# Kernel optimization log

Hardware: AMD Instinct MI355X
Metric: run time of the kernel (lower is better)

## Reference

```python
import jax, jax.numpy as jnp
import numpy as np
import math

N_NODES, CHANNELS, N_ELEM, N_FEAT = 4096, 128, 10, 128
LS_IN = [0, 1, 2]          # input irreps per channel: 0e+1o+2e -> dim 9
L_OUT = [0, 1]             # keep_irrep_out = {0e, 1o}
L12_MAX = 3                # cap on intermediate coupling
SLICES = {0: (0, 1), 1: (1, 4), 2: (4, 9)}
PATHS1 = [l for l in L_OUT if l in LS_IN]
PATHS2 = [(l1, l2, lo) for l1 in LS_IN for l2 in LS_IN for lo in L_OUT if abs(l1 - l2) <= lo <= l1 + l2]
T12_KEYS = [(l1, l2, l12) for l1 in LS_IN for l2 in LS_IN for l12 in range(abs(l1 - l2), min(l1 + l2, L12_MAX) + 1)]
PATHS3 = [(k, l3, lo) for k in T12_KEYS for l3 in LS_IN for lo in L_OUT if abs(k[2] - l3) <= lo <= k[2] + l3]

def _su2_cg(j1, m1, j2, m2, j3, m3):
    if m3 != m1 + m2:
        return 0.0
    f = math.factorial
    vmin = max(-j1 + j2 + m3, -j1 + m1, 0)
    vmax = min(j2 + j3 + m1, j3 - j1 + j2, j3 + m3)
    C = math.sqrt((2 * j3 + 1) * f(j3 + j1 - j2) * f(j3 - j1 + j2) * f(j1 + j2 - j3) * f(j3 + m3) * f(j3 - m3)
                  / (f(j1 + j2 + j3 + 1) * f(j1 - m1) * f(j1 + m1) * f(j2 - m2) * f(j2 + m2)))
    S = 0.0
    for v in range(vmin, vmax + 1):
        S += (-1) ** (v + j2 + m2) * f(j2 + j3 + m1 - v) * f(j1 - m1 + v) / (
            f(v) * f(j3 - j1 + j2 - v) * f(j3 + m3 - v) * f(v + j1 - j2 - m3))
    return C * S

def _c2r(l):
    # change of basis real -> complex spherical harmonics (e3nn convention)
    q = np.zeros((2 * l + 1, 2 * l + 1), dtype=np.complex128)
    for m in range(-l, 0):
        q[l + m, l + abs(m)] = 1.0 / math.sqrt(2)
        q[l + m, l - abs(m)] = -1j / math.sqrt(2)
    q[l, l] = 1.0
    for m in range(1, l + 1):
        q[l + m, l + abs(m)] = (-1) ** m / math.sqrt(2)
        q[l + m, l - abs(m)] = 1j * (-1) ** m / math.sqrt(2)
    return (-1j) ** l * q

_CG = {}
def real_cg(l1, l2, l3):
    key = (l1, l2, l3)
    if key not in _CG:
        Cc = np.zeros((2 * l1 + 1, 2 * l2 + 1, 2 * l3 + 1), dtype=np.complex128)
        for i, m1 in enumerate(range(-l1, l1 + 1)):
            for j, m2 in enumerate(range(-l2, l2 + 1)):
                for k, m3 in enumerate(range(-l3, l3 + 1)):
                    Cc[i, j, k] = _su2_cg(l1, m1, l2, m2, l3, m3)
        R = np.einsum('ij,kl,mn,ikn->jlm', _c2r(l1), _c2r(l2), np.conj(_c2r(l3).T), Cc)
        _CG[key] = np.real(R).astype(np.float32)
    return _CG[key]

def setup_inputs():
    key = jax.random.key(0)
    k = jax.random.split(key, 8)
    node_feats = jax.random.normal(k[0], (N_NODES, CHANNELS, 9), dtype=jnp.float32)
    species = jax.random.randint(k[1], (N_NODES,), 0, N_ELEM)
    w1 = jax.random.normal(k[2], (N_ELEM, len(PATHS1), CHANNELS), dtype=jnp.float32) / math.sqrt(len(PATHS1))
    w2 = jax.random.normal(k[3], (N_ELEM, len(PATHS2), CHANNELS), dtype=jnp.float32) / math.sqrt(len(PATHS2))
    w3 = jax.random.normal(k[4], (N_ELEM, len(PATHS3), CHANNELS), dtype=jnp.float32) / math.sqrt(len(PATHS3))
    lin_w0 = jax.random.normal(k[5], (CHANNELS, N_FEAT), dtype=jnp.float32)
    lin_w1 = jax.random.normal(k[6], (CHANNELS, N_FEAT), dtype=jnp.float32)
    return {"node_feats": node_feats, "w1": w1, "w2": w2, "w3": w3,
            "lin_w0": lin_w0, "lin_w1": lin_w1, "species": species}

def reference(node_feats, w1, w2, w3, lin_w0, lin_w1, species):
    n, c = node_feats.shape[:2]
    attrs = jax.nn.one_hot(species, N_ELEM, dtype=node_feats.dtype)
    A = {l: node_feats[..., SLICES[l][0]:SLICES[l][1]] for l in LS_IN}
    # element-dependent path weights per node
    w1n = jnp.einsum('ne,epc->npc', attrs, w1)
    w2n = jnp.einsum('ne,epc->npc', attrs, w2)
    w3n = jnp.einsum('ne,epc->npc', attrs, w3)
    B = {lo: jnp.zeros((n, c, 2 * lo + 1), node_feats.dtype) for lo in L_OUT}
    # correlation order 1
    for p, lo in enumerate(PATHS1):
        B[lo] = B[lo] + w1n[:, p, :, None] * A[lo]
    for p, (l1, l2, lo) in enumerate(PATHS2):
        cg = jnp.asarray(real_cg(l1, l2, lo))
        t = jnp.einsum('ijk,nci,ncj->nck', cg, A[l1], A[l2])
        B[lo] = B[lo] + w2n[:, p, :, None] * t
    T12 = {}
    for kk in T12_KEYS:
        l1, l2, l12 = kk
        T12[kk] = jnp.einsum('ijk,nci,ncj->nck', jnp.asarray(real_cg(l1, l2, l12)), A[l1], A[l2])
    for p, (kk, l3, lo) in enumerate(PATHS3):
        cg = jnp.asarray(real_cg(kk[2], l3, lo))
        t = jnp.einsum('ijk,nci,ncj->nck', cg, T12[kk], A[l3])
        B[lo] = B[lo] + w3n[:, p, :, None] * t
    # equivariant Linear: mix channel axis into num_features per output irrep
    s = 1.0 / math.sqrt(c)
    out0 = jnp.einsum('ncm,cf->nfm', B[0], lin_w0) * s
    out1 = jnp.einsum('ncm,cf->nfm', B[1], lin_w1) * s
    return jnp.concatenate([out0, out1], axis=-1)  # [N, F, 1+3]
```

## Files before the change

kernel.cpp:

```cpp
#include <hip/hip_runtime.h>
#include <utility>


#define NN 4096
#define NC 128
#define TN 2

template<typename F, int... Is>
__device__ __forceinline__ void sfor_impl(F&& f, std::integer_sequence<int, Is...>) {
  (f(std::integral_constant<int, Is>{}), ...);
}
template<int N, typename F>
__device__ __forceinline__ void sfor(F&& f) {
  sfor_impl((F&&)f, std::make_integer_sequence<int, N>{});
}

constexpr int T_L1c[19]  = {0,0,0,1,1,1,1,1,1,1,2,2,2,2,2,2,2,2,3};
constexpr int T_L2c[19]  = {0,1,2,0,1,1,1,2,2,2,0,1,1,1,2,2,2,2,2};
constexpr int T_L3c[19]  = {0,1,2,1,0,1,2,1,2,3,2,1,2,3,0,1,2,3,1};
constexpr int T_OFFc[19] = {0,1,10,35,44,53,80,125,170,245,350,375,420,495,600,625,700,825,1000};
constexpr int AOFFc[3]   = {0,1,4};

constexpr int P2_L1c[9]  = {0,0,1,1,1,1,2,2,2};
constexpr int P2_L2c[9]  = {0,1,0,1,1,2,1,2,2};
constexpr int P2_LOc[9]  = {0,1,1,0,1,1,1,0,1};
constexpr int P2_TBLc[9] = {0,1,3,4,5,7,11,14,15};

constexpr int K_L1c[18]  = {0,0,0,1,1,1,1,1,1,1,2,2,2,2,2,2,2,2};
constexpr int K_L2c[18]  = {0,1,2,0,1,1,1,2,2,2,0,1,1,1,2,2,2,2};
constexpr int K_L12c[18] = {0,1,2,1,0,1,2,1,2,3,2,1,2,3,0,1,2,3};

constexpr int P3_STARTc[19] = {0,2,6,9,13,15,19,22,26,29,30,33,37,40,41,43,47,50,51};
constexpr int P3_L3c[51] = {
  0,1,  0,1,1,2,  1,2,2,  0,1,1,2,  0,1,  0,1,1,2,  1,2,2,  0,1,1,2,  1,2,2,
  2,  1,2,2,  0,1,1,2,  1,2,2,  2,  0,1,  0,1,1,2,  1,2,2,  2 };
constexpr int P3_LOc[51] = {
  0,1,  1,0,1,1,  1,0,1,  1,0,1,1,  0,1,  1,0,1,1,  1,0,1,  1,0,1,1,  1,0,1,
  1,  1,0,1,  1,0,1,1,  1,0,1,  1,  0,1,  1,0,1,1,  1,0,1,  1 };
constexpr int P3_TBLc[51] = {
  0,1,  3,4,5,7,  11,14,15,  3,4,5,7,  0,1,  3,4,5,7,  11,14,15,  3,4,5,7,
  11,14,15,  18,  11,14,15,  3,4,5,7,  11,14,15,  18,  0,1,  3,4,5,7,
  11,14,15,  18 };

constexpr double cfact(int n) { double r = 1.0; for (int i = 2; i <= n; ++i) r *= i; return r; }
constexpr double csqrt(double x) {
  if (x <= 0.0) return 0.0;
  double r = x > 1.0 ? x : 1.0;
  for (int i = 0; i < 64; ++i) r = 0.5 * (r + x / r);
  return r;
}
constexpr double su2cg(int j1, int m1, int j2, int m2, int j3, int m3) {
  if (m3 != m1 + m2) return 0.0;
  int vmin = -j1 + j2 + m3; if (-j1 + m1 > vmin) vmin = -j1 + m1; if (vmin < 0) vmin = 0;
  int vmax = j2 + j3 + m1; if (j3 - j1 + j2 < vmax) vmax = j3 - j1 + j2; if (j3 + m3 < vmax) vmax = j3 + m3;
  double C = csqrt((2.0 * j3 + 1.0)
                   * cfact(j3 + j1 - j2) * cfact(j3 - j1 + j2) * cfact(j1 + j2 - j3)
                   * cfact(j3 + m3) * cfact(j3 - m3)
                   / (cfact(j1 + j2 + j3 + 1) * cfact(j1 - m1) * cfact(j1 + m1)
                      * cfact(j2 - m2) * cfact(j2 + m2)));
  double S = 0.0;
  for (int v = vmin; v <= vmax; ++v) {
    double sgn = ((v + j2 + m2) & 1) ? -1.0 : 1.0;
    S += sgn * cfact(j2 + j3 + m1 - v) * cfact(j1 - m1 + v)
         / (cfact(v) * cfact(j3 - j1 + j2 - v) * cfact(j3 + m3 - v) * cfact(v + j1 - j2 - m3));
  }
  return C * S;
}

struct Cx { double re, im; };
constexpr Cx cxmul(Cx a, Cx b) { return Cx{a.re * b.re - a.im * b.im, a.re * b.im + a.im * b.re}; }
struct Row { int cnt; int col[2]; Cx v[2]; };

constexpr Row c2r_row(int l, int r) {
  Row out{0, {0, 0}, {{0, 0}, {0, 0}}};
  constexpr double is2 = 0.70710678118654752440;
  const int m = r - l;
  if (m < 0) {
    out.cnt = 2;
    out.col[0] = l - m; out.v[0] = Cx{is2, 0.0};
    out.col[1] = l + m; out.v[1] = Cx{0.0, -is2};
  } else if (m == 0) {
    out.cnt = 1; out.col[0] = l; out.v[0] = Cx{1.0, 0.0};
  } else {
    const double sgn = (m & 1) ? -1.0 : 1.0;
    out.cnt = 2;
    out.col[0] = l + m; out.v[0] = Cx{sgn * is2, 0.0};
    out.col[1] = l - m; out.v[1] = Cx{0.0, sgn * is2};
  }
  const int ph = l & 3;
  for (int a = 0; a < out.cnt; ++a) {
    Cx v = out.v[a];
    out.v[a] = (ph == 0) ? v
             : (ph == 1) ? Cx{v.im, -v.re}
             : (ph == 2) ? Cx{-v.re, -v.im}
                         : Cx{-v.im, v.re};
  }
  return out;
}

struct CGAll { float v[1105]; };
constexpr CGAll make_cg() {
  CGAll R{};
  for (int t = 0; t < 19; ++t) {
    const int l1 = T_L1c[t], l2 = T_L2c[t], l3 = T_L3c[t], off = T_OFFc[t];
    const int d1 = 2 * l1 + 1, d2 = 2 * l2 + 1, d3 = 2 * l3 + 1;
    double tmp[175] = {};
    for (int i = 0; i < d1; ++i) {
      const int m1 = i - l1;
      const Row r1 = c2r_row(l1, i);
      for (int k = 0; k < d2; ++k) {
        const int m2 = k - l2, m3 = m1 + m2;
        if (m3 < -l3 || m3 > l3) continue;
        const double cc = su2cg(l1, m1, l2, m2, l3, m3);
        if (cc == 0.0) continue;
        const Row r2 = c2r_row(l2, k);
        const Row r3 = c2r_row(l3, m3 + l3);
        for (int a = 0; a < r1.cnt; ++a)
          for (int b = 0; b < r2.cnt; ++b) {
            const Cx q12 = cxmul(r1.v[a], r2.v[b]);
            for (int cdx = 0; cdx < r3.cnt; ++cdx) {
              const double re = q12.re * r3.v[cdx].re + q12.im * r3.v[cdx].im;
              tmp[(r1.col[a] * d2 + r2.col[b]) * d3 + r3.col[cdx]] += re * cc;
            }
          }
      }
    }
    const int sz = d1 * d2 * d3;
    for (int e = 0; e < sz; ++e) R.v[off + e] = (float)tmp[e];
  }
  return R;
}
constexpr CGAll CG_ALL = make_cg();

__global__ __launch_bounds__(256) void epb_main(
    const float* __restrict__ nf,
    const float* __restrict__ w1,
    const float* __restrict__ w2,
    const float* __restrict__ w3,
    const float* __restrict__ lw0,
    const float* __restrict__ lw1,
    const int*   __restrict__ species,
    float* __restrict__ out)
{
  __shared__ float4 Bsh[TN * NC];
  const int t  = threadIdx.x;
  const int nb = blockIdx.x * TN;
  const int c = t & 127, nl = t >> 7;
  const int s = species[nb + nl];

  const float* w1p = w1 + (size_t)s * 2  * NC + c;
  const float* w2p = w2 + (size_t)s * 9  * NC + c;
  const float* w3p = w3 + (size_t)s * 51 * NC + c;
  const float* ap  = nf + ((size_t)(nb + nl) * NC + c) * 9;

  float w3r[51];
  sfor<51>([&](auto P) { w3r[P.value] = w3p[P.value * NC]; });
  float w2r[9];
  sfor<9>([&](auto P) { w2r[P.value] = w2p[P.value * NC]; });
  float w1r0 = w1p[0], w1r1 = w1p[NC];
  float A[9];
  sfor<9>([&](auto I) { A[I.value] = ap[I.value]; });

  float B[4];
  B[0] = w1r0 * A[0];
  B[1] = w1r1 * A[1];
  B[2] = w1r1 * A[2];
  B[3] = w1r1 * A[3];

  sfor<9>([&](auto P) {
    constexpr int p  = P.value;
    constexpr int l1 = P2_L1c[p], l2 = P2_L2c[p], lo = P2_LOc[p];
    constexpr int d1 = 2 * l1 + 1, d2 = 2 * l2 + 1, dl = 2 * lo + 1;
    constexpr int off = T_OFFc[P2_TBLc[p]];
    const float w = w2r[p];
    sfor<dl>([&](auto Kk) {
      constexpr int k = Kk.value;
      float v = 0.f;
      sfor<d1>([&](auto I) {
        sfor<d2>([&](auto J) {
          constexpr float cgc = CG_ALL.v[off + (I.value * d2 + J.value) * dl + k];
          if constexpr (cgc != 0.0f) {
            constexpr int ia = AOFFc[l1] + I.value, ja = AOFFc[l2] + J.value;
            constexpr int x = ia < ja ? ia : ja, y = ia < ja ? ja : ia;
            v = fmaf(cgc, A[x] * A[y], v);
          }
        });
      });
      B[lo + k] = fmaf(w, v, B[lo + k]);
    });
  });

  sfor<18>([&](auto T) {
    constexpr int t2  = T.value;
    constexpr int l1  = K_L1c[t2], l2 = K_L2c[t2], l12 = K_L12c[t2];
    constexpr int d1  = 2 * l1 + 1, d2 = 2 * l2 + 1, d12 = 2 * l12 + 1;
    constexpr int off = T_OFFc[t2];
    float tt[d12];
    sfor<d12>([&](auto Kk) {
      constexpr int k = Kk.value;
      float v = 0.f;
      sfor<d1>([&](auto I) {
        sfor<d2>([&](auto J) {
          constexpr float cgc = CG_ALL.v[off + (I.value * d2 + J.value) * d12 + k];
          if constexpr (cgc != 0.0f) {
            constexpr int ia = AOFFc[l1] + I.value, ja = AOFFc[l2] + J.value;
            constexpr int x = ia < ja ? ia : ja, y = ia < ja ? ja : ia;
            v = fmaf(cgc, A[x] * A[y], v);
          }
        });
      });
      tt[k] = v;
    });
    constexpr int pcnt = P3_STARTc[t2 + 1] - P3_STARTc[t2];
    sfor<pcnt>([&](auto PP) {
      constexpr int p  = P3_STARTc[t2] + PP.value;
      constexpr int l3 = P3_L3c[p], lo = P3_LOc[p];
      constexpr int d3 = 2 * l3 + 1, dl = 2 * lo + 1;
      constexpr int off2 = T_OFFc[P3_TBLc[p]];
      const float w = w3r[p];
      sfor<dl>([&](auto M) {
        float v = 0.f;
        sfor<d12>([&](auto Kk) {
          sfor<d3>([&](auto J) {
            constexpr float cgc = CG_ALL.v[off2 + (Kk.value * d3 + J.value) * dl + M.value];
            if constexpr (cgc != 0.0f)
              v = fmaf(cgc, tt[Kk.value] * A[AOFFc[l3] + J.value], v);
          });
        });
        B[lo + M.value] = fmaf(w, v, B[lo + M.value]);
      });
    });
  });

  Bsh[nl * NC + c] = make_float4(B[0], B[1], B[2], B[3]);
  __syncthreads();

  const int fl = t & 127, g = t >> 7;
  const float* pa = lw0 + fl;
  const float* pb = lw1 + fl;
  const float4* bp = &Bsh[g * NC];

  float a0 = 0.f, a1 = 0.f, a2 = 0.f, a3 = 0.f;

  #pragma unroll 8
  for (int ch = 0; ch < NC; ++ch) {
    const float wa = pa[ch * NC];
    const float wb = pb[ch * NC];
    const float4 b = bp[ch];
    a0 = fmaf(b.x, wa, a0);
    a1 = fmaf(b.y, wb, a1);
    a2 = fmaf(b.z, wb, a2);
    a3 = fmaf(b.w, wb, a3);
  }

  const float s4 = 0.08838834764831845f;
  float4* out4 = reinterpret_cast<float4*>(out);
  out4[(size_t)(nb + g) * NC + fl] = make_float4(a0*s4, a1*s4, a2*s4, a3*s4);
}

extern "C" void kernel_launch(void* const* d_in, const int* in_sizes, int n_in,
                              void* d_out, int out_size, void* d_ws, size_t ws_size,
                              hipStream_t stream) {
  const float* nf  = (const float*)d_in[0];
  const float* w1  = (const float*)d_in[1];
  const float* w2  = (const float*)d_in[2];
  const float* w3  = (const float*)d_in[3];
  const float* lw0 = (const float*)d_in[4];
  const float* lw1 = (const float*)d_in[5];
  const int*   spc = (const int*)  d_in[6];
  float* out = (float*)d_out;
  (void)d_ws; (void)ws_size; (void)in_sizes; (void)n_in; (void)out_size;

  hipLaunchKernelGGL(epb_main, dim3(NN / TN), dim3(256), 0, stream,
                     nf, w1, w2, w3, lw0, lw1, spc, out);
}
```

Measured before the change: 107.3 us.

## Exploit CG exchange symmetry, pack weights, and split-K the channel linear

Uses CG exchange symmetry so only 13 canonical l1xl2 intermediates are computed and each feeds both its own and its swapped key's paths. Order-2 paths with swapped l1/l2 are merged by summing their weights. A pre-pass kernel packs w1/w2/w3 per element into float4 rows, so each thread loads its weights with 16 vector loads. The final channel-mixing linear is restructured so each thread computes four output features over a quarter of the channels with float4 weight loads, and the partials are reduced through shared memory. This adds an extra launch, an extra sync and more shared memory.

```diff
diff --git a/kernel.cpp b/kernel.cpp
--- a/kernel.cpp
+++ b/kernel.cpp
@@ -4,6 +4,7 @@
 
 #define NN 4096
 #define NC 128
+#define NE 10
 #define TN 2
 
 template<typename F, int... Is>
@@ -21,14 +22,21 @@
 constexpr int T_OFFc[19] = {0,1,10,35,44,53,80,125,170,245,350,375,420,495,600,625,700,825,1000};
 constexpr int AOFFc[3]   = {0,1,4};
 
-constexpr int P2_L1c[9]  = {0,0,1,1,1,1,2,2,2};
-constexpr int P2_L2c[9]  = {0,1,0,1,1,2,1,2,2};
-constexpr int P2_LOc[9]  = {0,1,1,0,1,1,1,0,1};
-constexpr int P2_TBLc[9] = {0,1,3,4,5,7,11,14,15};
+constexpr int P2U_L1c[7]  = {0,0,1,1,1,2,2};
+constexpr int P2U_L2c[7]  = {0,1,1,1,2,2,2};
+constexpr int P2U_LOc[7]  = {0,1,0,1,1,0,1};
+constexpr int P2U_TBLc[7] = {0,1,4,5,7,14,15};
+constexpr int P2U_WAc[7]  = {0,1,3,4,5,7,8};
+constexpr int P2U_WBc[7]  = {-1,2,-1,-1,6,-1,-1};
 
 constexpr int K_L1c[18]  = {0,0,0,1,1,1,1,1,1,1,2,2,2,2,2,2,2,2};
 constexpr int K_L2c[18]  = {0,1,2,0,1,1,1,2,2,2,0,1,1,1,2,2,2,2};
 constexpr int K_L12c[18] = {0,1,2,1,0,1,2,1,2,3,2,1,2,3,0,1,2,3};
+
+constexpr int   TT_CANONc[18] = {0,1,2,1,4,5,6,7,8,9,2,7,8,9,14,15,16,17};
+constexpr float TT_SGNc[18]   = {1,1,1,1,1,1,1,1,1,1,1,1,-1,1,1,1,1,1};
+constexpr int CANONc[13] = {0,1,2,4,5,6,7,8,9,14,15,16,17};
+constexpr int CONS2c[13] = {-1,3,10,-1,-1,-1,11,12,13,-1,-1,-1,-1};
 
 constexpr int P3_STARTc[19] = {0,2,6,9,13,15,19,22,26,29,30,33,37,40,41,43,47,50,51};
 constexpr int P3_L3c[51] = {
@@ -132,130 +140,208 @@
 }
 constexpr CGAll CG_ALL = make_cg();
 
+constexpr bool check_cg_sym() {
+  for (int t = 0; t < 18; ++t) {
+    const int tc = TT_CANONc[t];
+    if (tc == t) continue;
+    const int l1 = K_L1c[t], l2 = K_L2c[t], l12 = K_L12c[t];
+    const int d1 = 2*l1+1, d2 = 2*l2+1, d12 = 2*l12+1;
+    for (int i = 0; i < d1; ++i)
+      for (int j = 0; j < d2; ++j)
+        for (int k = 0; k < d12; ++k) {
+          float a = CG_ALL.v[T_OFFc[t]  + (i*d2 + j)*d12 + k];
+          float b = TT_SGNc[t] * CG_ALL.v[T_OFFc[tc] + (j*d1 + i)*d12 + k];
+          float d = a - b; if (d < 0) d = -d;
+          if (d > 1e-5f) return false;
+        }
+  }
+  return true;
+}
+static_assert(check_cg_sym(), "CG exchange symmetry violated");
+
+__global__ __launch_bounds__(256) void wt_pack(
+    const float* __restrict__ w1, const float* __restrict__ w2,
+    const float* __restrict__ w3, float4* __restrict__ wpack)
+{
+  const int tid = blockIdx.x * 256 + threadIdx.x;
+  if (tid >= NE * 16 * NC) return;
+  const int e = tid / (16 * NC);
+  const int r = tid % (16 * NC);
+  const int i = r / NC;
+  const int c = r % NC;
+  float v[4];
+  #pragma unroll
+  for (int j = 0; j < 4; ++j) {
+    const int p = i * 4 + j;
+    float x = 0.f;
+    if (p < 2)       x = w1[((size_t)e * 2  + p)        * NC + c];
+    else if (p < 11) x = w2[((size_t)e * 9  + (p - 2))  * NC + c];
+    else if (p < 62) x = w3[((size_t)e * 51 + (p - 11)) * NC + c];
+    v[j] = x;
+  }
+  wpack[tid] = make_float4(v[0], v[1], v[2], v[3]);
+}
+
 __global__ __launch_bounds__(256) void epb_main(
-    const float* __restrict__ nf,
-    const float* __restrict__ w1,
-    const float* __restrict__ w2,
-    const float* __restrict__ w3,
-    const float* __restrict__ lw0,
-    const float* __restrict__ lw1,
-    const int*   __restrict__ species,
+    const float*  __restrict__ nf,
+    const float4* __restrict__ wpack,
+    const float*  __restrict__ lw0,
+    const float*  __restrict__ lw1,
+    const int*    __restrict__ species,
     float* __restrict__ out)
 {
   __shared__ float4 Bsh[TN * NC];
+  __shared__ float4 psh[4 * TN * NC];
   const int t  = threadIdx.x;
   const int nb = blockIdx.x * TN;
-  const int c = t & 127, nl = t >> 7;
-  const int s = species[nb + nl];
-
-  const float* w1p = w1 + (size_t)s * 2  * NC + c;
-  const float* w2p = w2 + (size_t)s * 9  * NC + c;
-  const float* w3p = w3 + (size_t)s * 51 * NC + c;
-  const float* ap  = nf + ((size_t)(nb + nl) * NC + c) * 9;
-
-  float w3r[51];
-  sfor<51>([&](auto P) { w3r[P.value] = w3p[P.value * NC]; });
-  float w2r[9];
-  sfor<9>([&](auto P) { w2r[P.value] = w2p[P.value * NC]; });
-  float w1r0 = w1p[0], w1r1 = w1p[NC];
-  float A[9];
-  sfor<9>([&](auto I) { A[I.value] = ap[I.value]; });
-
-  float B[4];
-  B[0] = w1r0 * A[0];
-  B[1] = w1r1 * A[1];
-  B[2] = w1r1 * A[2];
-  B[3] = w1r1 * A[3];
-
-  sfor<9>([&](auto P) {
-    constexpr int p  = P.value;
-    constexpr int l1 = P2_L1c[p], l2 = P2_L2c[p], lo = P2_LOc[p];
-    constexpr int d1 = 2 * l1 + 1, d2 = 2 * l2 + 1, dl = 2 * lo + 1;
-    constexpr int off = T_OFFc[P2_TBLc[p]];
-    const float w = w2r[p];
-    sfor<dl>([&](auto Kk) {
-      constexpr int k = Kk.value;
-      float v = 0.f;
-      sfor<d1>([&](auto I) {
-        sfor<d2>([&](auto J) {
-          constexpr float cgc = CG_ALL.v[off + (I.value * d2 + J.value) * dl + k];
-          if constexpr (cgc != 0.0f) {
-            constexpr int ia = AOFFc[l1] + I.value, ja = AOFFc[l2] + J.value;
-            constexpr int x = ia < ja ? ia : ja, y = ia < ja ? ja : ia;
-            v = fmaf(cgc, A[x] * A[y], v);
-          }
-        });
+
+  {
+    const int c = t & 127, nl = t >> 7;
+    const int s = species[nb + nl];
+
+    float wr[64];
+    {
+      const float4* wp = wpack + ((size_t)s * 16) * NC + c;
+      sfor<16>([&](auto I) {
+        const float4 v = wp[I.value * NC];
+        wr[4*I.value+0] = v.x; wr[4*I.value+1] = v.y;
+        wr[4*I.value+2] = v.z; wr[4*I.value+3] = v.w;
       });
-      B[lo + k] = fmaf(w, v, B[lo + k]);
-    });
-  });
-
-  sfor<18>([&](auto T) {
-    constexpr int t2  = T.value;
-    constexpr int l1  = K_L1c[t2], l2 = K_L2c[t2], l12 = K_L12c[t2];
-    constexpr int d1  = 2 * l1 + 1, d2 = 2 * l2 + 1, d12 = 2 * l12 + 1;
-    constexpr int off = T_OFFc[t2];
-    float tt[d12];
-    sfor<d12>([&](auto Kk) {
-      constexpr int k = Kk.value;
-      float v = 0.f;
-      sfor<d1>([&](auto I) {
-        sfor<d2>([&](auto J) {
-          constexpr float cgc = CG_ALL.v[off + (I.value * d2 + J.value) * d12 + k];
-          if constexpr (cgc != 0.0f) {
-            constexpr int ia = AOFFc[l1] + I.value, ja = AOFFc[l2] + J.value;
-            constexpr int x = ia < ja ? ia : ja, y = ia < ja ? ja : ia;
-            v = fmaf(cgc, A[x] * A[y], v);
-          }
-        });
-      });
-      tt[k] = v;
-    });
-    constexpr int pcnt = P3_STARTc[t2 + 1] - P3_STARTc[t2];
-    sfor<pcnt>([&](auto PP) {
-      constexpr int p  = P3_STARTc[t2] + PP.value;
-      constexpr int l3 = P3_L3c[p], lo = P3_LOc[p];
-      constexpr int d3 = 2 * l3 + 1, dl = 2 * lo + 1;
-      constexpr int off2 = T_OFFc[P3_TBLc[p]];
-      const float w = w3r[p];
-      sfor<dl>([&](auto M) {
+    }
+    const float* ap = nf + ((size_t)(nb + nl) * NC + c) * 9;
+    float A[9];
+    sfor<9>([&](auto I) { A[I.value] = ap[I.value]; });
+
+    float B[4];
+    B[0] = wr[0] * A[0];
+    B[1] = wr[1] * A[1];
+    B[2] = wr[1] * A[2];
+    B[3] = wr[1] * A[3];
+
+    sfor<7>([&](auto P) {
+      constexpr int p  = P.value;
+      constexpr int l1 = P2U_L1c[p], l2 = P2U_L2c[p], lo = P2U_LOc[p];
+      constexpr int d1 = 2*l1+1, d2 = 2*l2+1, dl = 2*lo+1;
+      constexpr int off = T_OFFc[P2U_TBLc[p]];
+      float w = wr[2 + P2U_WAc[p]];
+      if constexpr (P2U_WBc[p] >= 0) w += wr[2 + P2U_WBc[p]];
+      sfor<dl>([&](auto Kk) {
+        constexpr int k = Kk.value;
         float v = 0.f;
-        sfor<d12>([&](auto Kk) {
-          sfor<d3>([&](auto J) {
-            constexpr float cgc = CG_ALL.v[off2 + (Kk.value * d3 + J.value) * dl + M.value];
-            if constexpr (cgc != 0.0f)
-              v = fmaf(cgc, tt[Kk.value] * A[AOFFc[l3] + J.value], v);
+        sfor<d1>([&](auto I) {
+          sfor<d2>([&](auto J) {
+            constexpr float cgc = CG_ALL.v[off + (I.value * d2 + J.value) * dl + k];
+            if constexpr (cgc != 0.0f) {
+              constexpr int ia = AOFFc[l1] + I.value, ja = AOFFc[l2] + J.value;
+              constexpr int x = ia < ja ? ia : ja, y = ia < ja ? ja : ia;
+              v = fmaf(cgc, A[x] * A[y], v);
+            }
           });
         });
-        B[lo + M.value] = fmaf(w, v, B[lo + M.value]);
+        B[lo + k] = fmaf(w, v, B[lo + k]);
       });
     });
-  });
-
-  Bsh[nl * NC + c] = make_float4(B[0], B[1], B[2], B[3]);
+
+    sfor<13>([&](auto CI) {
+      constexpr int tk  = CANONc[CI.value];
+      constexpr int l1  = K_L1c[tk], l2 = K_L2c[tk], l12 = K_L12c[tk];
+      constexpr int d1  = 2*l1+1, d2 = 2*l2+1, d12 = 2*l12+1;
+      constexpr int off = T_OFFc[tk];
+      float tt[d12];
+      sfor<d12>([&](auto Kk) {
+        constexpr int k = Kk.value;
+        float v = 0.f;
+        sfor<d1>([&](auto I) {
+          sfor<d2>([&](auto J) {
+            constexpr float cgc = CG_ALL.v[off + (I.value * d2 + J.value) * d12 + k];
+            if constexpr (cgc != 0.0f) {
+              constexpr int ia = AOFFc[l1] + I.value, ja = AOFFc[l2] + J.value;
+              constexpr int x = ia < ja ? ia : ja, y = ia < ja ? ja : ia;
+              v = fmaf(cgc, A[x] * A[y], v);
+            }
+          });
+        });
+        tt[k] = v;
+      });
+
+      auto consume = [&](auto TK, auto SG) {
+        constexpr int tkey = TK.value;
+        constexpr float sgn = (float)SG.value;
+        constexpr int pcnt = P3_STARTc[tkey + 1] - P3_STARTc[tkey];
+        sfor<pcnt>([&](auto PP) {
+          constexpr int p  = P3_STARTc[tkey] + PP.value;
+          constexpr int l3 = P3_L3c[p], lo = P3_LOc[p];
+          constexpr int d3 = 2*l3+1, dl = 2*lo+1;
+          constexpr int off2 = T_OFFc[P3_TBLc[p]];
+          const float w = wr[11 + p];
+          sfor<dl>([&](auto M) {
+            float v = 0.f;
+            sfor<d12>([&](auto Kk) {
+              sfor<d3>([&](auto J) {
+                constexpr float cgc = sgn * CG_ALL.v[off2 + (Kk.value * d3 + J.value) * dl + M.value];
+                if constexpr (cgc != 0.0f)
+                  v = fmaf(cgc, tt[Kk.value] * A[AOFFc[l3] + J.value], v);
+              });
+            });
+            B[lo + M.value] = fmaf(w, v, B[lo + M.value]);
+          });
+        });
+      };
+      consume(std::integral_constant<int, tk>{}, std::integral_constant<int, 1>{});
+      constexpr int td = CONS2c[CI.value];
+      if constexpr (td >= 0)
+        consume(std::integral_constant<int, td>{},
+                std::integral_constant<int, (int)TT_SGNc[td]>{});
+    });
+
+    Bsh[nl * NC + c] = make_float4(B[0], B[1], B[2], B[3]);
+  }
   __syncthreads();
 
-  const int fl = t & 127, g = t >> 7;
-  const float* pa = lw0 + fl;
-  const float* pb = lw1 + fl;
-  const float4* bp = &Bsh[g * NC];
-
-  float a0 = 0.f, a1 = 0.f, a2 = 0.f, a3 = 0.f;
-
-  #pragma unroll 8
-  for (int ch = 0; ch < NC; ++ch) {
-    const float wa = pa[ch * NC];
-    const float wb = pb[ch * NC];
-    const float4 b = bp[ch];
-    a0 = fmaf(b.x, wa, a0);
-    a1 = fmaf(b.y, wb, a1);
-    a2 = fmaf(b.z, wb, a2);
-    a3 = fmaf(b.w, wb, a3);
-  }
-
-  const float s4 = 0.08838834764831845f;
-  float4* out4 = reinterpret_cast<float4*>(out);
-  out4[(size_t)(nb + g) * NC + fl] = make_float4(a0*s4, a1*s4, a2*s4, a3*s4);
+  {
+    const int q  = t & 31;
+    const int g  = (t >> 5) & 1;
+    const int kp = t >> 6;
+    const float4* pa4 = reinterpret_cast<const float4*>(lw0) + q;
+    const float4* pb4 = reinterpret_cast<const float4*>(lw1) + q;
+    const float4* bp  = &Bsh[g * NC + kp * 32];
+
+    float4 of0{0,0,0,0}, of1{0,0,0,0}, of2{0,0,0,0}, of3{0,0,0,0};
+
+    #pragma unroll 4
+    for (int ch2 = 0; ch2 < 32; ++ch2) {
+      const int ch = kp * 32 + ch2;
+      const float4 wa = pa4[ch * 32];
+      const float4 wb = pb4[ch * 32];
+      const float4 b  = bp[ch2];
+      of0.x = fmaf(b.x, wa.x, of0.x); of0.y = fmaf(b.y, wb.x, of0.y);
+      of0.z = fmaf(b.z, wb.x, of0.z); of0.w = fmaf(b.w, wb.x, of0.w);
+      of1.x = fmaf(b.x, wa.y, of1.x); of1.y = fmaf(b.y, wb.y, of1.y);
+      of1.z = fmaf(b.z, wb.y, of1.z); of1.w = fmaf(b.w, wb.y, of1.w);
+      of2.x = fmaf(b.x, wa.z, of2.x); of2.y = fmaf(b.y, wb.z, of2.y);
+      of2.z = fmaf(b.z, wb.z, of2.z); of2.w = fmaf(b.w, wb.z, of2.w);
+      of3.x = fmaf(b.x, wa.w, of3.x); of3.y = fmaf(b.y, wb.w, of3.y);
+      of3.z = fmaf(b.z, wb.w, of3.z); of3.w = fmaf(b.w, wb.w, of3.w);
+    }
+    float4* pp = &psh[((kp * TN + g) * NC) + 4 * q];
+    pp[0] = of0; pp[1] = of1; pp[2] = of2; pp[3] = of3;
+  }
+  __syncthreads();
+
+  {
+    const int f = t & 127, g2 = t >> 7;
+    const float4 p0 = psh[((0 * TN + g2) * NC) + f];
+    const float4 p1 = psh[((1 * TN + g2) * NC) + f];
+    const float4 p2 = psh[((2 * TN + g2) * NC) + f];
+    const float4 p3 = psh[((3 * TN + g2) * NC) + f];
+    const float s4 = 0.08838834764831845f;
+    float4 r;
+    r.x = (p0.x + p1.x + p2.x + p3.x) * s4;
+    r.y = (p0.y + p1.y + p2.y + p3.y) * s4;
+    r.z = (p0.z + p1.z + p2.z + p3.z) * s4;
+    r.w = (p0.w + p1.w + p2.w + p3.w) * s4;
+    reinterpret_cast<float4*>(out)[(size_t)(nb + g2) * NC + f] = r;
+  }
 }
 
 extern "C" void kernel_launch(void* const* d_in, const int* in_sizes, int n_in,
@@ -269,8 +355,11 @@
   const float* lw1 = (const float*)d_in[5];
   const int*   spc = (const int*)  d_in[6];
   float* out = (float*)d_out;
-  (void)d_ws; (void)ws_size; (void)in_sizes; (void)n_in; (void)out_size;
-
+  float4* wpack = (float4*)d_ws;
+  (void)ws_size; (void)in_sizes; (void)n_in; (void)out_size;
+
+  hipLaunchKernelGGL(wt_pack, dim3((NE * 16 * NC + 255) / 256), dim3(256), 0, stream,
+                     w1, w2, w3, wpack);
   hipLaunchKernelGGL(epb_main, dim3(NN / TN), dim3(256), 0, stream,
-                     nf, w1, w2, w3, lw0, lw1, spc, out);
-}
+                     nf, wpack, lw0, lw1, spc, out);
+}
```

Result: faster. 105.0 us (-2.1%).
